# Performance work log

Hardware: AMD Instinct MI355X
Metric: run time of the kernel (lower is better)

## Reference

```python
import jax, jax.numpy as jnp
import numpy as np

B, S, D, H = 4, 2048, 512, 8
HD = D // H  # head_dim = 64


def setup_inputs() -> dict:
    key = jax.random.key(0)
    ks = jax.random.split(key, 11)
    sc = 1.0 / np.sqrt(D)
    inp = {
        "query": jax.random.normal(ks[0], (B, S, D), jnp.float32),
        "key": jax.random.normal(ks[1], (B, S, D), jnp.float32),
        "value": jax.random.normal(ks[2], (B, S, D), jnp.float32),
        "Wq": jax.random.normal(ks[3], (D, D), jnp.float32) * sc,
        "bq": jax.random.normal(ks[4], (D,), jnp.float32) * sc,
        "Wk": jax.random.normal(ks[5], (D, D), jnp.float32) * sc,
        "bk": jax.random.normal(ks[6], (D,), jnp.float32) * sc,
        "Wv": jax.random.normal(ks[7], (D, D), jnp.float32) * sc,
        "bv": jax.random.normal(ks[8], (D,), jnp.float32) * sc,
        "Wo": jax.random.normal(ks[9], (D, D), jnp.float32) * sc,
        "bo": jax.random.normal(ks[10], (D,), jnp.float32) * sc,
    }
    return inp


def reference(query, key, value, Wq, bq, Wk, bk, Wv, bv, Wo, bo):
    batch = query.shape[0]
    # Linear projections (x @ W + b)
    q = query @ Wq + bq
    k = key @ Wk + bk
    v = value @ Wv + bv
    # NOTE: original uses .view(B*H, -1, head_dim) — a raw row-major reshape
    # (interleaves seq and head dims). Replicated exactly with jnp.reshape.
    q = q.reshape(batch * H, -1, HD)
    k = k.reshape(batch * H, -1, HD)
    v = v.reshape(batch * H, -1, HD)
    # scores: [B*H, L, L], fully materialized as in the original bmm path
    scores = jnp.einsum("bqd,bkd->bqk", q, k) / jnp.sqrt(jnp.float32(HD))
    probs = jax.nn.softmax(scores, axis=-1)  # dropout=0.0 -> identity
    out = jnp.einsum("bqk,bkd->bqd", probs, v)
    out = out.reshape(batch, -1, D)
    out = out @ Wo + bo
    return out, probs
```

## Files before the change

### kernel.cpp

```cpp
#include <hip/hip_runtime.h>


typedef __attribute__((ext_vector_type(4))) float fvec4;
typedef __attribute__((ext_vector_type(4))) float f32x4;
typedef __attribute__((ext_vector_type(8))) short bf16x8;
typedef __attribute__((ext_vector_type(4))) short bf16x4;

typedef const __attribute__((address_space(1))) unsigned int* gas_t;
typedef __attribute__((address_space(3))) unsigned int* las_t;

__device__ inline void gl_lds16(const void* g, void* l) {
    __builtin_amdgcn_global_load_lds((gas_t)g, (las_t)l, 16, 0, 0);
}

__device__ inline unsigned short f2bf_rne(float x) {
    unsigned u = __builtin_bit_cast(unsigned, x);
    unsigned r = (u + 0x7FFFu + ((u >> 16) & 1u)) >> 16;
    return (unsigned short)r;
}
__device__ inline float bf2f(unsigned short h) {
    unsigned u = ((unsigned)h) << 16;
    return __builtin_bit_cast(float, u);
}

__device__ inline int fo4(int row, int ch) { return row * 32 + ((ch ^ ((row >> 1) & 3)) * 8); }

__global__ __launch_bounds__(256) void split3h(
    const float* __restrict__ X0, const float* __restrict__ X1, const float* __restrict__ X2,
    unsigned short* __restrict__ Hb)
{
    const float* X = blockIdx.z == 0 ? X0 : blockIdx.z == 1 ? X1 : X2;
    unsigned short* H = Hb + (long long)blockIdx.z * 4194304;
    const long long i = (long long)(blockIdx.x * 256 + threadIdx.x) * 8;
    fvec4 a = *(const fvec4*)(X + i);
    fvec4 b = *(const fvec4*)(X + i + 4);
    bf16x8 h;
#pragma unroll
    for (int j = 0; j < 4; j++) {
        h[j]     = (short)f2bf_rne(a[j]);
        h[4 + j] = (short)f2bf_rne(b[j]);
    }
    *(bf16x8*)(H + i) = h;
}

__global__ __launch_bounds__(256) void wtrans_split(
    const float* __restrict__ W0, const float* __restrict__ W1,
    const float* __restrict__ W2, const float* __restrict__ W3,
    unsigned short* __restrict__ TH, unsigned short* __restrict__ TL)
{
    const float* W = blockIdx.z == 0 ? W0 : blockIdx.z == 1 ? W1 : blockIdx.z == 2 ? W2 : W3;
    unsigned short* th = TH + (long long)blockIdx.z * 262144;
    unsigned short* tl = TL + (long long)blockIdx.z * 262144;
    __shared__ float t[32][33];
    const int x = threadIdx.x, y = threadIdx.y;
    const int n0 = blockIdx.x * 32, k0 = blockIdx.y * 32;
#pragma unroll
    for (int j = 0; j < 4; j++) t[y + 8 * j][x] = W[(long long)(k0 + y + 8 * j) * 512 + n0 + x];
    __syncthreads();
#pragma unroll
    for (int j = 0; j < 4; j++) {
        float v = t[x][y + 8 * j];
        unsigned short h = f2bf_rne(v);
        th[(long long)(n0 + y + 8 * j) * 512 + k0 + x] = h;
        tl[(long long)(n0 + y + 8 * j) * 512 + k0 + x] = f2bf_rne(v - bf2f(h));
    }
}

template <bool SPLIT_OUT>
__global__ __launch_bounds__(256) void gemm_2t(
    const unsigned short* __restrict__ AH, long long sAz,
    const unsigned short* __restrict__ BH, const unsigned short* __restrict__ BL, long long sBz,
    const float* __restrict__ b0, const float* __restrict__ b1, const float* __restrict__ b2,
    unsigned short* __restrict__ OH, float* __restrict__ OF, long long sOz)
{
    __shared__ __align__(16) unsigned short sAh[2][4096];
    __shared__ __align__(16) unsigned short sBh[2][4096];
    __shared__ __align__(16) unsigned short sBl[2][4096];

    const int tid = threadIdx.x, lane = tid & 63, wv = tid >> 6;
    const int z = blockIdx.z;
    AH += z * sAz; BH += z * sBz; BL += z * sBz;
    const float* bias = z == 0 ? b0 : z == 1 ? b1 : b2;
    const int row0 = blockIdx.x * 128, col0 = blockIdx.y * 128;
    const int wr = wv >> 1, wc = wv & 1;
    const int l15 = lane & 15, g = lane >> 4;

    const unsigned short* srcA  = AH + (long long)row0 * 512;
    const unsigned short* srcBh = BH + (long long)col0 * 512;
    const unsigned short* srcBl = BL + (long long)col0 * 512;
    const int srow = lane >> 2;
    const int csrc = (lane & 3) ^ ((lane >> 3) & 3);

    f32x4 acc[4][4];
#pragma unroll
    for (int a = 0; a < 4; a++)
#pragma unroll
        for (int b = 0; b < 4; b++)
#pragma unroll
            for (int r = 0; r < 4; r++) acc[a][b][r] = 0.f;

    auto stage = [&](int buf, int k0) {
#pragma unroll
        for (int e = 0; e < 6; e++) {
            const int idx = wv * 6 + e;
            const int t = idx >> 3, i = idx & 7;
            const unsigned short* s_ = t == 0 ? srcA : t == 1 ? srcBh : srcBl;
            unsigned short* d_ = t == 0 ? &sAh[0][0] : t == 1 ? &sBh[0][0] : &sBl[0][0];
            gl_lds16(s_ + (long long)(i * 16 + srow) * 512 + k0 + csrc * 8,
                     d_ + buf * 4096 + i * 512);
        }
    };

    stage(0, 0);
    __syncthreads();
    int cur = 0;
    for (int t = 0; t < 16; t++) {
        if (t < 15) stage(cur ^ 1, (t + 1) * 32);
        bf16x8 aHf[4];
#pragma unroll
        for (int rb = 0; rb < 4; rb++) {
            const int r = wr * 64 + rb * 16 + l15;
            aHf[rb] = *(const bf16x8*)&sAh[cur][fo4(r, g)];
        }
#pragma unroll
        for (int cb = 0; cb < 4; cb++) {
            const int rB = wc * 64 + cb * 16 + l15;
            bf16x8 bH = *(const bf16x8*)&sBh[cur][fo4(rB, g)];
            bf16x8 bL = *(const bf16x8*)&sBl[cur][fo4(rB, g)];
#pragma unroll
            for (int rb = 0; rb < 4; rb++) {
                acc[rb][cb] = __builtin_amdgcn_mfma_f32_16x16x32_bf16(aHf[rb], bH, acc[rb][cb], 0, 0, 0);
                acc[rb][cb] = __builtin_amdgcn_mfma_f32_16x16x32_bf16(aHf[rb], bL, acc[rb][cb], 0, 0, 0);
            }
        }
        __syncthreads();
        cur ^= 1;
    }

#pragma unroll
    for (int rb = 0; rb < 4; rb++) {
#pragma unroll
        for (int cb = 0; cb < 4; cb++) {
            const int col = col0 + wc * 64 + cb * 16 + l15;
#pragma unroll
            for (int rr = 0; rr < 4; rr++) {
                const long long row = row0 + wr * 64 + rb * 16 + g * 4 + rr;
                float val = acc[rb][cb][rr] + bias[col];
                if constexpr (SPLIT_OUT) {
                    (OH + z * sOz)[row * 512 + col] = f2bf_rne(val);
                } else {
                    (OF + z * sOz)[row * 512 + col] = val;
                }
            }
        }
    }
}

__global__ __launch_bounds__(256) void vtrans2(
    const unsigned short* __restrict__ vh, unsigned short* __restrict__ vt)
{
    __shared__ __align__(16) unsigned short t[64][80];
    const int tid = threadIdx.x;
    const int c = blockIdx.y;
    const int l0 = blockIdx.x * 64;
    const long long cb = (long long)c * 131072;
    const int rrow = tid >> 3, ccol = (tid & 7) * 8;
#pragma unroll
    for (int rr = 0; rr < 2; rr++)
        *(bf16x8*)&t[rrow + rr * 32][ccol] =
            *(const bf16x8*)(vh + cb + (long long)(l0 + rrow + rr * 32) * 64 + ccol);
    __syncthreads();
#pragma unroll
    for (int rr = 0; rr < 2; rr++) {
        const int hd = rrow + rr * 32;
        bf16x8 o;
#pragma unroll
        for (int q2 = 0; q2 < 8; q2++) o[q2] = (short)t[ccol + q2][hd];
        *(bf16x8*)(vt + cb + (long long)hd * 2048 + l0 + ccol) = o;
    }
}

__global__ __launch_bounds__(256) void fused_attn(
    const unsigned short* __restrict__ qh, const unsigned short* __restrict__ kh,
    const unsigned short* __restrict__ vt,
    float* __restrict__ probs, unsigned short* __restrict__ aoh)
{
    __shared__ __align__(16) unsigned short skh[64][80];
    __shared__ __align__(16) unsigned short svt[64][80];
    __shared__ __align__(16) unsigned short sP[4][16][68];

    const int tid = threadIdx.x, lane = tid & 63, wv = tid >> 6;

    const int orig = blockIdx.y * 32 + blockIdx.x;
    const int myid = (orig & 7) * 128 + (orig >> 3);
    const int c    = myid >> 5;
    const int row0 = (myid & 31) * 64;
    const long long cbase = (long long)c * 131072;

    const int l15 = lane & 15, g = lane >> 4, kk = g * 8;
    const int srow = tid >> 3;
    const int scol = (tid & 7) * 8;
    const int p_r0 = g * 4;

    const int arow = row0 + wv * 16 + l15;
    bf16x8 aH[2];
    {
        const unsigned short* qp = qh + cbase + (long long)arow * 64;
        aH[0] = *(const bf16x8*)(qp + kk);
        aH[1] = *(const bf16x8*)(qp + 32 + kk);
    }

    bf16x8 rkh[2], rvt[2];
    auto ld1 = [&](int j) {
        const long long ktb = cbase + (long long)j * 4096;
        const long long vtb = cbase + j * 64;
#pragma unroll
        for (int rr = 0; rr < 2; rr++) {
            const int r2 = srow + rr * 32;
            rkh[rr] = *(const bf16x8*)(kh + ktb + (long long)r2 * 64 + scol);
            rvt[rr] = *(const bf16x8*)(vt + vtb + (long long)r2 * 2048 + scol);
        }
    };
    auto st1 = [&]() {
#pragma unroll
        for (int rr = 0; rr < 2; rr++) {
            const int r2 = srow + rr * 32;
            *(bf16x8*)&skh[r2][scol] = rkh[rr];
            *(bf16x8*)&svt[r2][scol] = rvt[rr];
        }
    };
    auto ld2 = [&](int j) {
        const long long ktb = cbase + (long long)j * 4096;
#pragma unroll
        for (int rr = 0; rr < 2; rr++) {
            const int r2 = srow + rr * 32;
            rkh[rr] = *(const bf16x8*)(kh + ktb + (long long)r2 * 64 + scol);
        }
    };
    auto st2 = [&]() {
#pragma unroll
        for (int rr = 0; rr < 2; rr++) {
            const int r2 = srow + rr * 32;
            *(bf16x8*)&skh[r2][scol] = rkh[rr];
        }
    };

    f32x4 acc_o[4];
#pragma unroll
    for (int i = 0; i < 4; i++)
#pragma unroll
        for (int r = 0; r < 4; r++) acc_o[i][r] = 0.f;
    float rsum[4] = {0.f, 0.f, 0.f, 0.f};

    ld1(0);
    for (int j = 0; j < 32; j++) {
        __syncthreads();
        st1();
        if (j < 31) ld1(j + 1);
        __syncthreads();

        f32x4 s[4];
#pragma unroll
        for (int cb = 0; cb < 4; cb++)
#pragma unroll
            for (int r = 0; r < 4; r++) s[cb][r] = 0.f;
#pragma unroll
        for (int ks = 0; ks < 2; ks++) {
#pragma unroll
            for (int cb = 0; cb < 4; cb++) {
                bf16x8 bH = *(const bf16x8*)&skh[cb * 16 + l15][ks * 32 + kk];
                s[cb] = __builtin_amdgcn_mfma_f32_16x16x32_bf16(aH[ks], bH, s[cb], 0, 0, 0);
            }
        }
#pragma unroll
        for (int cb = 0; cb < 4; cb++) {
#pragma unroll
            for (int r = 0; r < 4; r++) {
                float p = __expf(s[cb][r] * 0.125f);
                rsum[r] += p;
                sP[wv][p_r0 + r][cb * 16 + l15] = f2bf_rne(p);
            }
        }
#pragma unroll
        for (int ks = 0; ks < 2; ks++) {
            bf16x4 p0 = *(const bf16x4*)&sP[wv][l15][ks * 32 + kk];
            bf16x4 p1 = *(const bf16x4*)&sP[wv][l15][ks * 32 + kk + 4];
            bf16x8 pa;
#pragma unroll
            for (int q2 = 0; q2 < 4; q2++) { pa[q2] = p0[q2]; pa[4 + q2] = p1[q2]; }
#pragma unroll
            for (int co = 0; co < 4; co++) {
                bf16x8 bV = *(const bf16x8*)&svt[co * 16 + l15][ks * 32 + kk];
                acc_o[co] = __builtin_amdgcn_mfma_f32_16x16x32_bf16(pa, bV, acc_o[co], 0, 0, 0);
            }
        }
    }

#pragma unroll
    for (int r = 0; r < 4; r++) {
        float s = rsum[r];
        s += __shfl_xor(s, 1, 64);
        s += __shfl_xor(s, 2, 64);
        s += __shfl_xor(s, 4, 64);
        s += __shfl_xor(s, 8, 64);
        rsum[r] = 1.f / s;
    }

#pragma unroll
    for (int co = 0; co < 4; co++) {
#pragma unroll
        for (int r = 0; r < 4; r++) {
            const long long oi = cbase + (long long)(row0 + wv * 16 + p_r0 + r) * 64 + co * 16 + l15;
            aoh[oi] = f2bf_rne(acc_o[co][r] * rsum[r]);
        }
    }

    ld2(0);
    for (int j = 0; j < 32; j++) {
        __syncthreads();
        st2();
        if (j < 31) ld2(j + 1);
        __syncthreads();

        f32x4 s[4];
#pragma unroll
        for (int cb = 0; cb < 4; cb++)
#pragma unroll
            for (int r = 0; r < 4; r++) s[cb][r] = 0.f;
#pragma unroll
        for (int ks = 0; ks < 2; ks++) {
#pragma unroll
            for (int cb = 0; cb < 4; cb++) {
                bf16x8 bH = *(const bf16x8*)&skh[cb * 16 + l15][ks * 32 + kk];
                s[cb] = __builtin_amdgcn_mfma_f32_16x16x32_bf16(aH[ks], bH, s[cb], 0, 0, 0);
            }
        }
        float* pb = probs + (long long)c * 4194304 +
                    (long long)(row0 + wv * 16 + p_r0) * 2048 + j * 64;
#pragma unroll
        for (int cb = 0; cb < 4; cb++) {
#pragma unroll
            for (int r = 0; r < 4; r++) {
                pb[(long long)r * 2048 + cb * 16 + l15] = __expf(s[cb][r] * 0.125f) * rsum[r];
            }
        }
    }
}

extern "C" void kernel_launch(void* const* d_in, const int* in_sizes, int n_in,
                              void* d_out, int out_size, void* d_ws, size_t ws_size,
                              hipStream_t stream)
{
    const float* query = (const float*)d_in[0];
    const float* key_  = (const float*)d_in[1];
    const float* value = (const float*)d_in[2];
    const float* Wq = (const float*)d_in[3];
    const float* bq = (const float*)d_in[4];
    const float* Wk = (const float*)d_in[5];
    const float* bk = (const float*)d_in[6];
    const float* Wv = (const float*)d_in[7];
    const float* bv = (const float*)d_in[8];
    const float* Wo = (const float*)d_in[9];
    const float* bo = (const float*)d_in[10];

    float* out   = (float*)d_out;
    float* probs = out + 4194304LL;

    const long long MiB = 1LL << 20;
    char* w = (char*)d_ws;
    unsigned short* QKVH = (unsigned short*)(w + 0 * MiB);
    unsigned short* WTH  = (unsigned short*)(w + 24 * MiB);
    unsigned short* WTL  = (unsigned short*)(w + 26 * MiB);
    unsigned short* VT   = (unsigned short*)(w + 28 * MiB);
    unsigned short* AOH  = (unsigned short*)(w + 36 * MiB);
    unsigned short* XH   = (unsigned short*)(w + 44 * MiB);

    split3h<<<dim3(2048, 1, 3), 256, 0, stream>>>(query, key_, value, XH);
    wtrans_split<<<dim3(16, 16, 4), dim3(32, 8, 1), 0, stream>>>(Wq, Wk, Wv, Wo, WTH, WTL);

    gemm_2t<true><<<dim3(64, 4, 3), 256, 0, stream>>>(
        XH, 4194304, WTH, WTL, 262144, bq, bk, bv,
        QKVH, nullptr, 4194304);

    vtrans2<<<dim3(32, 32, 1), 256, 0, stream>>>(QKVH + 2 * 4194304LL, VT);

    fused_attn<<<dim3(32, 32, 1), 256, 0, stream>>>(
        QKVH, QKVH + 4194304LL, VT, probs, AOH);

    gemm_2t<false><<<dim3(64, 4, 1), 256, 0, stream>>>(
        AOH, 0, WTH + 3 * 262144LL, WTL + 3 * 262144LL, 0, bo, bo, bo,
        nullptr, out, 0);
}
```

Before: 325.1 us.

## Read K and V^T MFMA operands directly from global memory, dropping LDS staging

Removes the shared-memory staging of K and V^T tiles and the register double-buffering, so each wave loads its MFMA B operands straight from global memory (through the caches). This drops two block-wide barriers per iteration and the LDS store and load traffic. In exchange each of the four waves fetches the same K/V tile on its own, quadrupling global and L2 requests, and loads are no longer prefetched one tile ahead, so latency may be exposed.

```diff
diff --git a/kernel.cpp b/kernel.cpp
--- a/kernel.cpp
+++ b/kernel.cpp
@@ -185,8 +185,6 @@
     const unsigned short* __restrict__ vt,
     float* __restrict__ probs, unsigned short* __restrict__ aoh)
 {
-    __shared__ __align__(16) unsigned short skh[64][80];
-    __shared__ __align__(16) unsigned short svt[64][80];
     __shared__ __align__(16) unsigned short sP[4][16][68];
 
     const int tid = threadIdx.x, lane = tid & 63, wv = tid >> 6;
@@ -198,8 +196,6 @@
     const long long cbase = (long long)c * 131072;
 
     const int l15 = lane & 15, g = lane >> 4, kk = g * 8;
-    const int srow = tid >> 3;
-    const int scol = (tid & 7) * 8;
     const int p_r0 = g * 4;
 
     const int arow = row0 + wv * 16 + l15;
@@ -210,40 +206,8 @@
         aH[1] = *(const bf16x8*)(qp + 32 + kk);
     }
 
-    bf16x8 rkh[2], rvt[2];
-    auto ld1 = [&](int j) {
-        const long long ktb = cbase + (long long)j * 4096;
-        const long long vtb = cbase + j * 64;
-#pragma unroll
-        for (int rr = 0; rr < 2; rr++) {
-            const int r2 = srow + rr * 32;
-            rkh[rr] = *(const bf16x8*)(kh + ktb + (long long)r2 * 64 + scol);
-            rvt[rr] = *(const bf16x8*)(vt + vtb + (long long)r2 * 2048 + scol);
-        }
-    };
-    auto st1 = [&]() {
-#pragma unroll
-        for (int rr = 0; rr < 2; rr++) {
-            const int r2 = srow + rr * 32;
-            *(bf16x8*)&skh[r2][scol] = rkh[rr];
-            *(bf16x8*)&svt[r2][scol] = rvt[rr];
-        }
-    };
-    auto ld2 = [&](int j) {
-        const long long ktb = cbase + (long long)j * 4096;
-#pragma unroll
-        for (int rr = 0; rr < 2; rr++) {
-            const int r2 = srow + rr * 32;
-            rkh[rr] = *(const bf16x8*)(kh + ktb + (long long)r2 * 64 + scol);
-        }
-    };
-    auto st2 = [&]() {
-#pragma unroll
-        for (int rr = 0; rr < 2; rr++) {
-            const int r2 = srow + rr * 32;
-            *(bf16x8*)&skh[r2][scol] = rkh[rr];
-        }
-    };
+    const unsigned short* kb = kh + cbase;
+    const unsigned short* vb = vt + cbase;
 
     f32x4 acc_o[4];
 #pragma unroll
@@ -252,12 +216,8 @@
         for (int r = 0; r < 4; r++) acc_o[i][r] = 0.f;
     float rsum[4] = {0.f, 0.f, 0.f, 0.f};
 
-    ld1(0);
     for (int j = 0; j < 32; j++) {
-        __syncthreads();
-        st1();
-        if (j < 31) ld1(j + 1);
-        __syncthreads();
+        const unsigned short* kt = kb + (long long)j * 4096;
 
         f32x4 s[4];
 #pragma unroll
@@ -268,7 +228,7 @@
         for (int ks = 0; ks < 2; ks++) {
 #pragma unroll
             for (int cb = 0; cb < 4; cb++) {
-                bf16x8 bH = *(const bf16x8*)&skh[cb * 16 + l15][ks * 32 + kk];
+                bf16x8 bH = *(const bf16x8*)(kt + (long long)(cb * 16 + l15) * 64 + ks * 32 + kk);
                 s[cb] = __builtin_amdgcn_mfma_f32_16x16x32_bf16(aH[ks], bH, s[cb], 0, 0, 0);
             }
         }
@@ -290,7 +250,8 @@
             for (int q2 = 0; q2 < 4; q2++) { pa[q2] = p0[q2]; pa[4 + q2] = p1[q2]; }
 #pragma unroll
             for (int co = 0; co < 4; co++) {
-                bf16x8 bV = *(const bf16x8*)&svt[co * 16 + l15][ks * 32 + kk];
+                bf16x8 bV = *(const bf16x8*)(vb + (long long)(co * 16 + l15) * 2048 +
+                                             j * 64 + ks * 32 + kk);
                 acc_o[co] = __builtin_amdgcn_mfma_f32_16x16x32_bf16(pa, bV, acc_o[co], 0, 0, 0);
             }
         }
@@ -315,12 +276,8 @@
         }
     }
 
-    ld2(0);
     for (int j = 0; j < 32; j++) {
-        __syncthreads();
-        st2();
-        if (j < 31) ld2(j + 1);
-        __syncthreads();
+        const unsigned short* kt = kb + (long long)j * 4096;
 
         f32x4 s[4];
 #pragma unroll
@@ -331,7 +288,7 @@
         for (int ks = 0; ks < 2; ks++) {
 #pragma unroll
             for (int cb = 0; cb < 4; cb++) {
-                bf16x8 bH = *(const bf16x8*)&skh[cb * 16 + l15][ks * 32 + kk];
+                bf16x8 bH = *(const bf16x8*)(kt + (long long)(cb * 16 + l15) * 64 + ks * 32 + kk);
                 s[cb] = __builtin_amdgcn_mfma_f32_16x16x32_bf16(aH[ks], bH, s[cb], 0, 0, 0);
             }
         }
```

After: 557.9 us. 71.6% more time.

## Widen attention blocks to 512 threads and vectorize transposed probs stores

Applied to the files above, without the earlier changes.

Doubles the attention block to 512 threads covering 128 query rows, so each K/V tile staged in LDS is reused by twice as many waves and each thread loads one row instead of two. In the second pass the MFMA operands are swapped so each lane holds four consecutive key columns of one query row. The row normalizer is redistributed with shuffles, which lets the probs output be written as 16-byte float4 stores instead of scalar strided stores. The cost is fewer blocks in the grid and a higher register and LDS demand per block, which can lower occupancy.

```diff
diff --git a/kernel.cpp b/kernel.cpp
--- a/kernel.cpp
+++ b/kernel.cpp
@@ -180,21 +180,22 @@
     }
 }
 
-__global__ __launch_bounds__(256) void fused_attn(
+__global__ __launch_bounds__(512) void fused_attn(
     const unsigned short* __restrict__ qh, const unsigned short* __restrict__ kh,
     const unsigned short* __restrict__ vt,
     float* __restrict__ probs, unsigned short* __restrict__ aoh)
 {
-    __shared__ __align__(16) unsigned short skh[64][80];
-    __shared__ __align__(16) unsigned short svt[64][80];
-    __shared__ __align__(16) unsigned short sP[4][16][68];
+    __shared__ __align__(16) char smem[35840];
+    unsigned short (*skh)[72] = (unsigned short(*)[72])smem;
+    unsigned short (*svt)[72] = (unsigned short(*)[72])(smem + 9216);
+    unsigned short (*sP)[16][68] = (unsigned short(*)[16][68])(smem + 18432);
 
     const int tid = threadIdx.x, lane = tid & 63, wv = tid >> 6;
 
-    const int orig = blockIdx.y * 32 + blockIdx.x;
-    const int myid = (orig & 7) * 128 + (orig >> 3);
-    const int c    = myid >> 5;
-    const int row0 = (myid & 31) * 64;
+    const int orig = blockIdx.y * 16 + blockIdx.x;
+    const int myid = (orig & 7) * 64 + (orig >> 3);
+    const int c    = myid >> 4;
+    const int row0 = (myid & 15) * 128;
     const long long cbase = (long long)c * 131072;
 
     const int l15 = lane & 15, g = lane >> 4, kk = g * 8;
@@ -210,39 +211,20 @@
         aH[1] = *(const bf16x8*)(qp + 32 + kk);
     }
 
-    bf16x8 rkh[2], rvt[2];
+    bf16x8 rkh, rvt_;
     auto ld1 = [&](int j) {
-        const long long ktb = cbase + (long long)j * 4096;
-        const long long vtb = cbase + j * 64;
-#pragma unroll
-        for (int rr = 0; rr < 2; rr++) {
-            const int r2 = srow + rr * 32;
-            rkh[rr] = *(const bf16x8*)(kh + ktb + (long long)r2 * 64 + scol);
-            rvt[rr] = *(const bf16x8*)(vt + vtb + (long long)r2 * 2048 + scol);
-        }
+        rkh  = *(const bf16x8*)(kh + cbase + (long long)(j * 64 + srow) * 64 + scol);
+        rvt_ = *(const bf16x8*)(vt + cbase + (long long)srow * 2048 + j * 64 + scol);
     };
     auto st1 = [&]() {
-#pragma unroll
-        for (int rr = 0; rr < 2; rr++) {
-            const int r2 = srow + rr * 32;
-            *(bf16x8*)&skh[r2][scol] = rkh[rr];
-            *(bf16x8*)&svt[r2][scol] = rvt[rr];
-        }
+        *(bf16x8*)&skh[srow][scol] = rkh;
+        *(bf16x8*)&svt[srow][scol] = rvt_;
     };
     auto ld2 = [&](int j) {
-        const long long ktb = cbase + (long long)j * 4096;
-#pragma unroll
-        for (int rr = 0; rr < 2; rr++) {
-            const int r2 = srow + rr * 32;
-            rkh[rr] = *(const bf16x8*)(kh + ktb + (long long)r2 * 64 + scol);
-        }
+        rkh = *(const bf16x8*)(kh + cbase + (long long)(j * 64 + srow) * 64 + scol);
     };
     auto st2 = [&]() {
-#pragma unroll
-        for (int rr = 0; rr < 2; rr++) {
-            const int r2 = srow + rr * 32;
-            *(bf16x8*)&skh[r2][scol] = rkh[rr];
-        }
+        *(bf16x8*)&skh[srow][scol] = rkh;
     };
 
     f32x4 acc_o[4];
@@ -315,7 +297,17 @@
         }
     }
 
+    const int srcl = (l15 >> 2) << 4;
+    float t0 = __shfl(rsum[0], srcl, 64);
+    float t1 = __shfl(rsum[1], srcl, 64);
+    float t2 = __shfl(rsum[2], srcl, 64);
+    float t3 = __shfl(rsum[3], srcl, 64);
+    float ta = (l15 & 1) ? t1 : t0;
+    float tb = (l15 & 1) ? t3 : t2;
+    const float rsum_q = (l15 & 2) ? tb : ta;
+
     ld2(0);
+    float* pq = probs + (long long)c * 4194304 + (long long)(row0 + wv * 16 + l15) * 2048;
     for (int j = 0; j < 32; j++) {
         __syncthreads();
         st2();
@@ -331,18 +323,16 @@
         for (int ks = 0; ks < 2; ks++) {
 #pragma unroll
             for (int cb = 0; cb < 4; cb++) {
-                bf16x8 bH = *(const bf16x8*)&skh[cb * 16 + l15][ks * 32 + kk];
-                s[cb] = __builtin_amdgcn_mfma_f32_16x16x32_bf16(aH[ks], bH, s[cb], 0, 0, 0);
-            }
-        }
-        float* pb = probs + (long long)c * 4194304 +
-                    (long long)(row0 + wv * 16 + p_r0) * 2048 + j * 64;
+                bf16x8 bK = *(const bf16x8*)&skh[cb * 16 + l15][ks * 32 + kk];
+                s[cb] = __builtin_amdgcn_mfma_f32_16x16x32_bf16(bK, aH[ks], s[cb], 0, 0, 0);
+            }
+        }
 #pragma unroll
         for (int cb = 0; cb < 4; cb++) {
-#pragma unroll
-            for (int r = 0; r < 4; r++) {
-                pb[(long long)r * 2048 + cb * 16 + l15] = __expf(s[cb][r] * 0.125f) * rsum[r];
-            }
+            fvec4 v;
+#pragma unroll
+            for (int r = 0; r < 4; r++) v[r] = __expf(s[cb][r] * 0.125f) * rsum_q;
+            *(fvec4*)(pq + j * 64 + cb * 16 + (g << 2)) = v;
         }
     }
 }
@@ -384,7 +374,7 @@
 
     vtrans2<<<dim3(32, 32, 1), 256, 0, stream>>>(QKVH + 2 * 4194304LL, VT);
 
-    fused_attn<<<dim3(32, 32, 1), 256, 0, stream>>>(
+    fused_attn<<<dim3(16, 32, 1), 512, 0, stream>>>(
         QKVH, QKVH + 4194304LL, VT, probs, AOH);
 
     gemm_2t<false><<<dim3(64, 4, 1), 256, 0, stream>>>(
```

New measurement: 327.9 us. Within noise of the previous version (+0.9%).
